# Performance work log

Measured on AMD Instinct MI355X. Metric: run time of the kernel, lower is better.

The kernel has to match this reference:

```python
import jax, jax.numpy as jnp
import numpy as np

EPS = 1e-3  # Keras LayerNormalization default epsilon


def setup_inputs() -> dict:
    key = jax.random.key(0)
    ks = jax.random.split(key, 10)
    B, S, D, U = 4, 4096, 1024, 1024
    sc_in = 1.0 / np.sqrt(D)
    sc_u = 1.0 / np.sqrt(U)
    return {
        "inputs": jax.random.normal(ks[0], (B, S, D), dtype=jnp.float32),
        "w1": jax.random.normal(ks[1], (D, U), dtype=jnp.float32) * sc_in,
        "b1": jnp.zeros((U,), dtype=jnp.float32),
        "w2": jax.random.normal(ks[2], (U, U), dtype=jnp.float32) * sc_u,
        "b2": jnp.zeros((U,), dtype=jnp.float32),
        "wg": jax.random.normal(ks[3], (D, U), dtype=jnp.float32) * sc_in,
        "bg": jnp.zeros((U,), dtype=jnp.float32),
        "ws": jax.random.normal(ks[4], (D, U), dtype=jnp.float32) * sc_in,
        "bs": jnp.zeros((U,), dtype=jnp.float32),
        "gamma": jnp.ones((U,), dtype=jnp.float32),
        "beta": jnp.zeros((U,), dtype=jnp.float32),
    }


def reference(inputs, w1, b1, w2, b2, wg, bg, ws, bs, gamma, beta):
    # hidden branch: Dense(relu) -> (dropout inactive at inference) -> Dense
    h = jax.nn.relu(jnp.einsum('bsd,du->bsu', inputs, w1) + b1)
    x = jnp.einsum('bsu,uv->bsv', h, w2) + b2
    # gate on raw inputs
    g = jax.nn.sigmoid(jnp.einsum('bsd,du->bsu', inputs, wg) + bg)
    # skip projection
    s = jnp.einsum('bsd,du->bsu', inputs, ws) + bs
    y = x * g + s
    # LayerNormalization over last axis (Keras default eps=1e-3)
    mu = jnp.mean(y, axis=-1, keepdims=True)
    var = jnp.mean(jnp.square(y - mu), axis=-1, keepdims=True)
    return (y - mu) * jax.lax.rsqrt(var + EPS) * gamma + beta
```

## Files before the change

kernel.cpp:

```cpp
#include <hip/hip_runtime.h>
#include <hip/hip_bf16.h>

typedef short short8 __attribute__((ext_vector_type(8)));
typedef float f32x4 __attribute__((ext_vector_type(4)));

#define M_TOT 16384
#define NDIM  1024
#define BK 32
#define NT (NDIM / BK)

static __device__ __forceinline__ unsigned short f2bf(float f) {
  unsigned int u = __builtin_bit_cast(unsigned int, f);
  unsigned int r = (u + 0x7fffu + ((u >> 16) & 1u)) >> 16;
  return (unsigned short)r;
}
static __device__ __forceinline__ float bf2f(unsigned short u) {
  return __builtin_bit_cast(float, ((unsigned int)u) << 16);
}

#define CLB() asm volatile("" ::: "memory")
#define VMW(N) asm volatile("s_waitcnt vmcnt(" #N ")" ::: "memory")
#define BAR() do { CLB(); __builtin_amdgcn_s_barrier(); CLB(); } while (0)

__global__ __launch_bounds__(256) void cast_in(const float* __restrict__ in,
                                               unsigned short* __restrict__ out,
                                               int n4) {
  int i = blockIdx.x * 256 + threadIdx.x;
  if (i >= n4) return;
  float4 v = reinterpret_cast<const float4*>(in)[i];
  ushort4 o;
  o.x = f2bf(v.x); o.y = f2bf(v.y); o.z = f2bf(v.z); o.w = f2bf(v.w);
  reinterpret_cast<ushort4*>(out)[i] = o;
}

__global__ __launch_bounds__(256) void tcast4(
    const float* __restrict__ w1, const float* __restrict__ w2,
    const float* __restrict__ wg, const float* __restrict__ ws,
    unsigned short* __restrict__ W1t, unsigned short* __restrict__ W2t,
    unsigned short* __restrict__ Wgt, unsigned short* __restrict__ Wst) {
  const int z = blockIdx.z;
  const float* src = (z == 0) ? w1 : (z == 1) ? w2 : (z == 2) ? wg : ws;
  unsigned short* dst = (z == 0) ? W1t : (z == 1) ? W2t : (z == 2) ? Wgt : Wst;
  __shared__ unsigned short tile[32][33];
  int bx = blockIdx.x * 32, by = blockIdx.y * 32;
  int x = threadIdx.x & 31, y = threadIdx.x >> 5;
#pragma unroll
  for (int i = 0; i < 32; i += 8)
    tile[y + i][x] = f2bf(src[(size_t)(by + y + i) * NDIM + bx + x]);
  __syncthreads();
#pragma unroll
  for (int i = 0; i < 32; i += 8)
    dst[(size_t)(bx + y + i) * NDIM + by + x] = tile[x][y + i];
}

__global__ __launch_bounds__(512, 2) void trigemm(
    const unsigned short* __restrict__ A,
    const unsigned short* __restrict__ W1t,
    const unsigned short* __restrict__ Wgt,
    const unsigned short* __restrict__ Wst,
    const float* __restrict__ b1,
    const float* __restrict__ bg,
    const float* __restrict__ bs,
    unsigned short* __restrict__ H,
    unsigned short* __restrict__ G,
    unsigned short* __restrict__ S) {
  __shared__ __align__(16) unsigned short lds[2][20480];

  const int tid = threadIdx.x;
  const int lane = tid & 63;
  const int wave = tid >> 6;
  const int wm = wave >> 1;
  const int wn = wave & 1;
  const int lr = lane & 15;
  const int lk = lane >> 4;

  const int id = blockIdx.x;
  const int xcd = id & 7;
  const int slot = id >> 3;
  const int rblk = xcd + 8 * (slot >> 3);
  const int cblk = slot & 7;
  const int m0 = rblk * 256, n0 = cblk * 128;

  const unsigned short* gA = A + (size_t)m0 * NDIM;
  const unsigned short* gW[3] = {W1t + (size_t)n0 * NDIM, Wgt + (size_t)n0 * NDIM,
                                 Wst + (size_t)n0 * NDIM};

  f32x4 acc[3][4][4] = {};

  auto stage = [&](int buf, int kt) {
#pragma unroll
    for (int q = 0; q < 5; ++q) {
      int cid = q * 512 + tid;
      const unsigned short* g;
      if (q < 2) {
        int row = cid >> 2;
        int c = (cid & 3) ^ ((row >> 1) & 3);
        g = gA + (size_t)row * NDIM + kt * BK + c * 8;
      } else {
        int local = cid - 1024 - (q - 2) * 512 + (q - 2) * 512;
        local = cid - 1024;
        int w = q - 2;
        int lrow = local & 511;
        int row = lrow >> 2;
        int c = (lrow & 3) ^ ((row >> 1) & 3);
        g = gW[w] + (size_t)row * NDIM + kt * BK + c * 8;
      }
      unsigned short* l = &lds[buf][0] + (size_t)(q * 512 + (tid & ~63)) * 8;
      __builtin_amdgcn_global_load_lds(
          (__attribute__((address_space(1))) void*)g,
          (__attribute__((address_space(3))) void*)l, 16, 0, 0);
    }
  };

  auto compute = [&](int buf) {
    short8 af[4];
#pragma unroll
    for (int mi = 0; mi < 4; ++mi) {
      int row = wm * 64 + mi * 16 + lr;
      int cs = lk ^ ((row >> 1) & 3);
      af[mi] = *reinterpret_cast<const short8*>(&lds[buf][row * 32 + cs * 8]);
    }
#pragma unroll
    for (int w = 0; w < 3; ++w) {
      short8 bf[4];
#pragma unroll
      for (int nj = 0; nj < 4; ++nj) {
        int row = wn * 64 + nj * 16 + lr;
        int cs = lk ^ ((row >> 1) & 3);
        bf[nj] = *reinterpret_cast<const short8*>(
            &lds[buf][8192 + w * 4096 + row * 32 + cs * 8]);
      }
      __builtin_amdgcn_s_setprio(1);
#pragma unroll
      for (int mi = 0; mi < 4; ++mi)
#pragma unroll
        for (int nj = 0; nj < 4; ++nj)
          acc[w][mi][nj] = __builtin_amdgcn_mfma_f32_16x16x32_bf16(
              af[mi], bf[nj], acc[w][mi][nj], 0, 0, 0);
      __builtin_amdgcn_s_setprio(0);
    }
  };

  stage(0, 0);
  for (int t = 0; t < NT; ++t) {
    const int cur = t & 1;
    if (t + 1 < NT) {
      stage(cur ^ 1, t + 1);
      VMW(5);
    } else {
      VMW(0);
    }
    BAR();
    compute(cur);
    BAR();
  }

  const int crow0 = m0 + wm * 64;
  const int ccol0 = n0 + wn * 64;
#pragma unroll
  for (int w = 0; w < 3; ++w) {
    const float* bptr = (w == 0) ? b1 : (w == 1) ? bg : bs;
    unsigned short* optr = (w == 0) ? H : (w == 1) ? G : S;
#pragma unroll
    for (int mi = 0; mi < 4; ++mi) {
#pragma unroll
      for (int nj = 0; nj < 4; ++nj) {
        int row = crow0 + mi * 16 + (lk << 2);
        int col = ccol0 + nj * 16 + lr;
        float bc = bptr[col];
#pragma unroll
        for (int r = 0; r < 4; ++r) {
          float v = acc[w][mi][nj][r] + bc;
          if (w == 0) v = fmaxf(v, 0.f);
          else if (w == 1) v = 1.f / (1.f + __expf(-v));
          optr[(size_t)(row + r) * NDIM + col] = f2bf(v);
        }
      }
    }
  }
}

__global__ __launch_bounds__(512, 2) void gemm_y(
    const unsigned short* __restrict__ A,
    const unsigned short* __restrict__ Bt,
    const float* __restrict__ bias,
    unsigned short* __restrict__ O,
    const unsigned short* __restrict__ G,
    const unsigned short* __restrict__ S) {
  __shared__ __align__(16) unsigned short lds[4][2][256][BK];

  const int tid = threadIdx.x;
  const int lane = tid & 63;
  const int wave = tid >> 6;
  const int wm = wave >> 2;
  const int wn = wave & 3;

  const int id = blockIdx.x;
  const int xcd = id & 7;
  const int slot0 = id >> 3;
  const int rblk = xcd + 8 * (slot0 >> 2);
  const int cblk = slot0 & 3;
  const int m0 = rblk * 256, n0 = cblk * 256;

  const unsigned short* gA = A + (size_t)m0 * NDIM;
  const unsigned short* gB = Bt + (size_t)n0 * NDIM;

  f32x4 acc[8][4] = {};

  auto stage = [&](int slot, int kt) {
#pragma unroll
    for (int q = 0; q < 4; ++q) {
      int cid = q * 512 + tid;
      int mat = q >> 1;
      int local = cid & 1023;
      int row = local >> 2;
      int c = (local & 3) ^ ((row >> 1) & 3);
      const unsigned short* g =
          (mat ? gB : gA) + (size_t)row * NDIM + kt * BK + c * 8;
      unsigned short* l = &lds[slot][mat][0][0] +
                          (size_t)((q * 512 + (tid & ~63)) & 1023) * 8;
      __builtin_amdgcn_global_load_lds(
          (__attribute__((address_space(1))) void*)g,
          (__attribute__((address_space(3))) void*)l, 16, 0, 0);
    }
  };

  auto compute = [&](int slot) {
    short8 af[8], bf[4];
#pragma unroll
    for (int nj = 0; nj < 4; ++nj) {
      int row = wn * 64 + nj * 16 + (lane & 15);
      int cs = (lane >> 4) ^ ((row >> 1) & 3);
      bf[nj] = *reinterpret_cast<const short8*>(&lds[slot][1][row][cs * 8]);
    }
#pragma unroll
    for (int mi = 0; mi < 8; ++mi) {
      int row = wm * 128 + mi * 16 + (lane & 15);
      int cs = (lane >> 4) ^ ((row >> 1) & 3);
      af[mi] = *reinterpret_cast<const short8*>(&lds[slot][0][row][cs * 8]);
    }
    __builtin_amdgcn_s_setprio(1);
#pragma unroll
    for (int mi = 0; mi < 8; ++mi)
#pragma unroll
      for (int nj = 0; nj < 4; ++nj)
        acc[mi][nj] = __builtin_amdgcn_mfma_f32_16x16x32_bf16(
            af[mi], bf[nj], acc[mi][nj], 0, 0, 0);
    __builtin_amdgcn_s_setprio(0);
  };

  stage(0, 0);
  stage(1, 1);
  stage(2, 2);
  VMW(8);
  BAR();

#pragma unroll 4
  for (int t = 0; t < NT - 4; ++t) {
    stage((t + 3) & 3, t + 3);
    compute(t & 3);
    VMW(8);
    BAR();
  }
  stage(3, 31);
  compute(0);
  VMW(8);
  BAR();
  compute(1);
  VMW(4);
  BAR();
  compute(2);
  VMW(0);
  BAR();
  compute(3);

  const int crow0 = m0 + wm * 128;
  const int ccol0 = n0 + wn * 64;
#pragma unroll
  for (int mi = 0; mi < 8; ++mi) {
#pragma unroll
    for (int nj = 0; nj < 4; ++nj) {
      int row = crow0 + mi * 16 + ((lane >> 4) << 2);
      int col = ccol0 + nj * 16 + (lane & 15);
      float bc = bias[col];
#pragma unroll
      for (int r = 0; r < 4; ++r) {
        float v = acc[mi][nj][r] + bc;
        size_t idx = (size_t)(row + r) * NDIM + col;
        O[idx] = f2bf(v * bf2f(G[idx]) + bf2f(S[idx]));
      }
    }
  }
}

__global__ __launch_bounds__(256) void layernorm_bf(
    const unsigned short* __restrict__ Ybf, float* __restrict__ Out,
    const float* __restrict__ gamma, const float* __restrict__ beta) {
  const int tid = threadIdx.x;
  const unsigned short* y = Ybf + (size_t)blockIdx.x * NDIM;
  ushort4 u = reinterpret_cast<const ushort4*>(y)[tid];
  float v0 = bf2f(u.x), v1 = bf2f(u.y), v2 = bf2f(u.z), v3 = bf2f(u.w);
  float s1 = v0 + v1 + v2 + v3;
  float s2 = v0 * v0 + v1 * v1 + v2 * v2 + v3 * v3;
#pragma unroll
  for (int o = 32; o > 0; o >>= 1) {
    s1 += __shfl_down(s1, o, 64);
    s2 += __shfl_down(s2, o, 64);
  }
  __shared__ float red[8];
  int wave = tid >> 6, lane = tid & 63;
  if (lane == 0) { red[wave] = s1; red[wave + 4] = s2; }
  __syncthreads();
  float S1 = red[0] + red[1] + red[2] + red[3];
  float S2 = red[4] + red[5] + red[6] + red[7];
  float mu = S1 * (1.f / NDIM);
  float var = S2 * (1.f / NDIM) - mu * mu;
  float inv = rsqrtf(var + 1e-3f);
  float4 gm = reinterpret_cast<const float4*>(gamma)[tid];
  float4 bt = reinterpret_cast<const float4*>(beta)[tid];
  float4 o;
  o.x = (v0 - mu) * inv * gm.x + bt.x;
  o.y = (v1 - mu) * inv * gm.y + bt.y;
  o.z = (v2 - mu) * inv * gm.z + bt.z;
  o.w = (v3 - mu) * inv * gm.w + bt.w;
  reinterpret_cast<float4*>(Out + (size_t)blockIdx.x * NDIM)[tid] = o;
}

extern "C" void kernel_launch(void* const* d_in, const int* in_sizes, int n_in,
                              void* d_out, int out_size, void* d_ws, size_t ws_size,
                              hipStream_t stream) {
  const float* inp = (const float*)d_in[0];
  const float* w1 = (const float*)d_in[1];
  const float* b1 = (const float*)d_in[2];
  const float* w2 = (const float*)d_in[3];
  const float* b2 = (const float*)d_in[4];
  const float* wg = (const float*)d_in[5];
  const float* bg = (const float*)d_in[6];
  const float* wsk = (const float*)d_in[7];
  const float* bs = (const float*)d_in[8];
  const float* gamma = (const float*)d_in[9];
  const float* beta = (const float*)d_in[10];

  char* p = (char*)d_ws;
  const size_t act_bf16 = (size_t)M_TOT * NDIM * 2;
  const size_t w_bf16 = (size_t)NDIM * NDIM * 2;
  unsigned short* Ain = (unsigned short*)p; p += act_bf16;
  unsigned short* H   = (unsigned short*)p; p += act_bf16;
  unsigned short* G   = (unsigned short*)p; p += act_bf16;
  unsigned short* S   = (unsigned short*)p; p += act_bf16;
  unsigned short* Ybf = (unsigned short*)p; p += act_bf16;
  unsigned short* W1t = (unsigned short*)p; p += w_bf16;
  unsigned short* W2t = (unsigned short*)p; p += w_bf16;
  unsigned short* Wgt = (unsigned short*)p; p += w_bf16;
  unsigned short* Wst = (unsigned short*)p; p += w_bf16;

  cast_in<<<(M_TOT * NDIM / 4 + 255) / 256, 256, 0, stream>>>(inp, Ain, M_TOT * NDIM / 4);
  tcast4<<<dim3(32, 32, 4), 256, 0, stream>>>(w1, w2, wg, wsk, W1t, W2t, Wgt, Wst);

  trigemm<<<(M_TOT / 256) * (NDIM / 128), 512, 0, stream>>>(
      Ain, W1t, Wgt, Wst, b1, bg, bs, H, G, S);
  gemm_y<<<(M_TOT / 256) * (NDIM / 256), 512, 0, stream>>>(H, W2t, b2, Ybf, G, S);
  layernorm_bf<<<M_TOT, 256, 0, stream>>>(Ybf, (float*)d_out, gamma, beta);
}
```

Baseline: 189.2 us.

## Shrink gemm_y tile to 256x128 with double-buffered LDS pipeline

Changes the second GEMM from 256x256 tiles with a 4-slot prefetch pipeline to 256x128 tiles with a simple two-buffer pipeline. Waves are rearranged as 4x2 so each accumulates a 64x64 block, which halves accumulator registers and doubles the grid to 512 blocks. The intent is better occupancy and load balance across CUs. In exchange there is less operand reuse per loaded byte, a shallower prefetch that hides less latency, and an extra barrier per k-step. It also removes a redundant line in trigemm.

```diff
diff --git a/kernel.cpp b/kernel.cpp
--- a/kernel.cpp
+++ b/kernel.cpp
@@ -97,8 +97,7 @@
         int c = (cid & 3) ^ ((row >> 1) & 3);
         g = gA + (size_t)row * NDIM + kt * BK + c * 8;
       } else {
-        int local = cid - 1024 - (q - 2) * 512 + (q - 2) * 512;
-        local = cid - 1024;
+        int local = cid - 1024;
         int w = q - 2;
         int lrow = local & 511;
         int row = lrow >> 2;
@@ -187,61 +186,67 @@
     unsigned short* __restrict__ O,
     const unsigned short* __restrict__ G,
     const unsigned short* __restrict__ S) {
-  __shared__ __align__(16) unsigned short lds[4][2][256][BK];
+  __shared__ __align__(16) unsigned short lds[2][12288];
 
   const int tid = threadIdx.x;
   const int lane = tid & 63;
   const int wave = tid >> 6;
-  const int wm = wave >> 2;
-  const int wn = wave & 3;
+  const int wm = wave >> 1;
+  const int wn = wave & 1;
+  const int lr = lane & 15;
+  const int lk = lane >> 4;
 
   const int id = blockIdx.x;
   const int xcd = id & 7;
-  const int slot0 = id >> 3;
-  const int rblk = xcd + 8 * (slot0 >> 2);
-  const int cblk = slot0 & 3;
-  const int m0 = rblk * 256, n0 = cblk * 256;
+  const int slot = id >> 3;
+  const int rblk = xcd + 8 * (slot >> 3);
+  const int cblk = slot & 7;
+  const int m0 = rblk * 256, n0 = cblk * 128;
 
   const unsigned short* gA = A + (size_t)m0 * NDIM;
   const unsigned short* gB = Bt + (size_t)n0 * NDIM;
 
-  f32x4 acc[8][4] = {};
-
-  auto stage = [&](int slot, int kt) {
-#pragma unroll
-    for (int q = 0; q < 4; ++q) {
+  f32x4 acc[4][4] = {};
+
+  auto stage = [&](int buf, int kt) {
+#pragma unroll
+    for (int q = 0; q < 3; ++q) {
       int cid = q * 512 + tid;
-      int mat = q >> 1;
-      int local = cid & 1023;
-      int row = local >> 2;
-      int c = (local & 3) ^ ((row >> 1) & 3);
-      const unsigned short* g =
-          (mat ? gB : gA) + (size_t)row * NDIM + kt * BK + c * 8;
-      unsigned short* l = &lds[slot][mat][0][0] +
-                          (size_t)((q * 512 + (tid & ~63)) & 1023) * 8;
+      const unsigned short* g;
+      if (q < 2) {
+        int row = cid >> 2;
+        int c = (cid & 3) ^ ((row >> 1) & 3);
+        g = gA + (size_t)row * NDIM + kt * BK + c * 8;
+      } else {
+        int local = cid - 1024;
+        int row = local >> 2;
+        int c = (local & 3) ^ ((row >> 1) & 3);
+        g = gB + (size_t)row * NDIM + kt * BK + c * 8;
+      }
+      unsigned short* l = &lds[buf][0] + (size_t)(q * 512 + (tid & ~63)) * 8;
       __builtin_amdgcn_global_load_lds(
           (__attribute__((address_space(1))) void*)g,
           (__attribute__((address_space(3))) void*)l, 16, 0, 0);
     }
   };
 
-  auto compute = [&](int slot) {
-    short8 af[8], bf[4];
+  auto compute = [&](int buf) {
+    short8 af[4], bf[4];
+#pragma unroll
+    for (int mi = 0; mi < 4; ++mi) {
+      int row = wm * 64 + mi * 16 + lr;
+      int cs = lk ^ ((row >> 1) & 3);
+      af[mi] = *reinterpret_cast<const short8*>(&lds[buf][row * 32 + cs * 8]);
+    }
 #pragma unroll
     for (int nj = 0; nj < 4; ++nj) {
-      int row = wn * 64 + nj * 16 + (lane & 15);
-      int cs = (lane >> 4) ^ ((row >> 1) & 3);
-      bf[nj] = *reinterpret_cast<const short8*>(&lds[slot][1][row][cs * 8]);
-    }
-#pragma unroll
-    for (int mi = 0; mi < 8; ++mi) {
-      int row = wm * 128 + mi * 16 + (lane & 15);
-      int cs = (lane >> 4) ^ ((row >> 1) & 3);
-      af[mi] = *reinterpret_cast<const short8*>(&lds[slot][0][row][cs * 8]);
+      int row = wn * 64 + nj * 16 + lr;
+      int cs = lk ^ ((row >> 1) & 3);
+      bf[nj] = *reinterpret_cast<const short8*>(&lds[buf][8192 + row * 32 + cs * 8]);
     }
     __builtin_amdgcn_s_setprio(1);
 #pragma unroll
-    for (int mi = 0; mi < 8; ++mi)
+    for (int mi = 0; mi < 4; ++mi)
 #pragma unroll
       for (int nj = 0; nj < 4; ++nj)
         acc[mi][nj] = __builtin_amdgcn_mfma_f32_16x16x32_bf16(
@@ -250,38 +255,27 @@
   };
 
   stage(0, 0);
-  stage(1, 1);
-  stage(2, 2);
-  VMW(8);
-  BAR();
-
-#pragma unroll 4
-  for (int t = 0; t < NT - 4; ++t) {
-    stage((t + 3) & 3, t + 3);
-    compute(t & 3);
-    VMW(8);
+  for (int t = 0; t < NT; ++t) {
+    const int cur = t & 1;
+    if (t + 1 < NT) {
+      stage(cur ^ 1, t + 1);
+      VMW(3);
+    } else {
+      VMW(0);
+    }
     BAR();
-  }
-  stage(3, 31);
-  compute(0);
-  VMW(8);
-  BAR();
-  compute(1);
-  VMW(4);
-  BAR();
-  compute(2);
-  VMW(0);
-  BAR();
-  compute(3);
-
-  const int crow0 = m0 + wm * 128;
+    compute(cur);
+    BAR();
+  }
+
+  const int crow0 = m0 + wm * 64;
   const int ccol0 = n0 + wn * 64;
 #pragma unroll
-  for (int mi = 0; mi < 8; ++mi) {
+  for (int mi = 0; mi < 4; ++mi) {
 #pragma unroll
     for (int nj = 0; nj < 4; ++nj) {
-      int row = crow0 + mi * 16 + ((lane >> 4) << 2);
-      int col = ccol0 + nj * 16 + (lane & 15);
+      int row = crow0 + mi * 16 + (lk << 2);
+      int col = ccol0 + nj * 16 + lr;
       float bc = bias[col];
 #pragma unroll
       for (int r = 0; r < 4; ++r) {
@@ -359,6 +353,6 @@
 
   trigemm<<<(M_TOT / 256) * (NDIM / 128), 512, 0, stream>>>(
       Ain, W1t, Wgt, Wst, b1, bg, bs, H, G, S);
-  gemm_y<<<(M_TOT / 256) * (NDIM / 256), 512, 0, stream>>>(H, W2t, b2, Ybf, G, S);
+  gemm_y<<<(M_TOT / 256) * (NDIM / 128), 512, 0, stream>>>(H, W2t, b2, Ybf, G, S);
   layernorm_bf<<<M_TOT, 256, 0, stream>>>(Ybf, (float*)d_out, gamma, beta);
 }
```

Measured after the change: 191.7 us. Within noise of the previous version (+1.3%).
